# Performance work log

Hardware: AMD Instinct MI355X
Metric: run time of the kernel (lower is better)

## Reference

```python
import jax, jax.numpy as jnp
import numpy as np

N_E = 8192
E_DIM = 64
BETA = 0.25
N_TOKENS = 32768


def setup_inputs() -> dict:
    key = jax.random.key(0)
    k1, k2 = jax.random.split(key)
    x = jax.random.normal(k1, (N_TOKENS, E_DIM), dtype=jnp.float32)
    # nn.Embedding weight initialized uniform(-1/n_e, 1/n_e)
    codebook = jax.random.uniform(k2, (N_E, E_DIM), dtype=jnp.float32,
                                  minval=-1.0 / N_E, maxval=1.0 / N_E)
    return {"x": x, "codebook": codebook, "start": 0, "end": N_E, "use_sk": 0}


def reference(x, codebook, start, end, use_sk):
    # use_sk=0 -> argmin branch (sinkhorn branch calls external helper, not exercised)
    latent = x.reshape(-1, E_DIM)                       # [N, D]
    cb = codebook[start:end]                            # [K, D]
    # squared euclidean distances: ||z||^2 + ||e||^2 - 2 z.e
    d = (jnp.sum(latent * latent, axis=1, keepdims=True)
         + jnp.sum(cb * cb, axis=1)[None, :]
         - 2.0 * jnp.einsum('nd,kd->nk', latent, cb))   # [N, K]
    indices = jnp.argmin(d, axis=-1) + start            # [N]
    x_q = codebook[indices].reshape(x.shape)            # gather
    sg = jax.lax.stop_gradient
    commitment_loss = jnp.mean((sg(x_q) - x) ** 2)
    codebook_loss = jnp.mean((x_q - sg(x)) ** 2)
    loss = codebook_loss + BETA * commitment_loss
    x_q_st = x + sg(x_q - x)                            # straight-through estimator
    indices = indices.reshape(x.shape[:-1])
    return x_q_st, loss, indices
```

## Files before the change

### kernel.cpp

```cpp
#include <hip/hip_runtime.h>
#include <math.h>


#define N_E    8192
#define EDIM   64
#define NTOK   32768
#define NELEM  (NTOK * EDIM)
#define CSZ    32
#define WINDOW 3e-4f
#define TTOK   256
#define TCODE  1024
#define SROW   72
#define TOKB   16
#define CCAP   64
#define KCAP   320

typedef __attribute__((ext_vector_type(8)))  short          short8;
typedef __attribute__((ext_vector_type(8)))  unsigned short ushort8v;
typedef __attribute__((ext_vector_type(16))) float          f32x16;

__device__ __forceinline__ unsigned short f2bf(float f) {
  unsigned int u = __float_as_uint(f);
  return (unsigned short)((u + 0x7FFFu + ((u >> 16) & 1u)) >> 16);
}
__device__ __forceinline__ unsigned short f2h(float f) {
  union { _Float16 h; unsigned short u; } cv; cv.h = (_Float16)f; return cv.u;
}
__device__ __forceinline__ float h2f(unsigned short b) {
  union { _Float16 h; unsigned short u; } cv; cv.u = b; return (float)cv.h;
}
__device__ __forceinline__ float max16(const f32x16 a) {
  float m = fmaxf(fmaxf(a[0], a[1]), a[2]);
  m = fmaxf(fmaxf(m, a[3]),  a[4]);
  m = fmaxf(fmaxf(m, a[5]),  a[6]);
  m = fmaxf(fmaxf(m, a[7]),  a[8]);
  m = fmaxf(fmaxf(m, a[9]),  a[10]);
  m = fmaxf(fmaxf(m, a[11]), a[12]);
  m = fmaxf(fmaxf(m, a[13]), a[14]);
  return fmaxf(m, a[15]);
}
__device__ __forceinline__ float sx_of(const float4* xl4) {
#pragma clang fp contract(off)
  float a0=0,a1=0,a2=0,a3=0,a4=0,a5=0,a6=0,a7=0;
#pragma unroll
  for (int i = 0; i < 8; ++i) {
    float4 pA = xl4[2*i], pB = xl4[2*i+1];
    a0 += pA.x * pA.x; a1 += pA.y * pA.y; a2 += pA.z * pA.z; a3 += pA.w * pA.w;
    a4 += pB.x * pB.x; a5 += pB.y * pB.y; a6 += pB.z * pB.z; a7 += pB.w * pB.w;
  }
  return ((a0+a1) + (a2+a3)) + ((a4+a5) + (a6+a7));
}

__global__ __launch_bounds__(256) void vq_sc(const float* __restrict__ cb,
                                             float* __restrict__ sc,
                                             unsigned short* __restrict__ cbf) {
#pragma clang fp contract(off)
  int r = blockIdx.x * 256 + threadIdx.x;
  const float4* c4 = (const float4*)(cb + (size_t)r * EDIM);
  float sval = sx_of(c4);
  sc[r] = sval;
  unsigned short* dst = cbf + (size_t)r * EDIM;
#pragma unroll
  for (int h = 0; h < 8; ++h) {
    float4 fA = c4[2*h], fB = c4[2*h+1];
    ushort8v o = {f2bf(fA.x), f2bf(fA.y), f2bf(fA.z), f2bf(fA.w),
                  f2bf(fB.x), f2bf(fB.y), f2bf(fB.z), f2bf(fB.w)};
    *(ushort8v*)&dst[h * 8] = o;
  }
}

__global__ __launch_bounds__(256, 3) void vq_pass1(
    const float* __restrict__ x, const unsigned short* __restrict__ cbf,
    unsigned int* __restrict__ cand,
    const int* __restrict__ p_start, const int* __restrict__ p_end) {
  __shared__ unsigned short Cs[128 * SROW];
  int tid = threadIdx.x;
  int tb = blockIdx.x;
  int cbk = blockIdx.y;
  int s = *p_start, e = *p_end;

  int lane = tid & 63, wv = tid >> 6;
  int half = lane >> 5, ln = lane & 31;
  int tokbase = wv * 64;

  const ushort8v* cg0 = (const ushort8v*)(cbf + (size_t)cbk * TCODE * EDIM);
#pragma unroll
  for (int p = 0; p < 4; ++p) {
    int idx = tid + p * 256;
    int row = idx >> 3, h = idx & 7;
    *(ushort8v*)&Cs[row * SROW + h * 8] = cg0[idx];
  }

  short8 bfr[2][4];
#pragma unroll
  for (int tg = 0; tg < 2; ++tg) {
    const float* xrow =
        x + (size_t)(tb * TTOK + tokbase + tg * 32 + ln) * EDIM + half * 8;
#pragma unroll
    for (int ks = 0; ks < 4; ++ks) {
      float4 fA = *(const float4*)(xrow + ks * 16);
      float4 fB = *(const float4*)(xrow + ks * 16 + 4);
      short8 v = {(short)f2bf(fA.x), (short)f2bf(fA.y), (short)f2bf(fA.z),
                  (short)f2bf(fA.w), (short)f2bf(fB.x), (short)f2bf(fB.y),
                  (short)f2bf(fB.z), (short)f2bf(fB.w)};
      bfr[tg][ks] = v;
    }
  }
  __syncthreads();

  unsigned s0=~0u,s1=~0u,s2=~0u,s3=~0u,s4=~0u,s5=~0u,s6=~0u,s7=~0u,s8=~0u;
  unsigned m0=0,m1=0,m2=0,m3=0,m4=0,m5=0,m6=0,m7=0,m8=0;
  unsigned bmap = 0u;
  float lm0 = INFINITY, lm1 = INFINITY;

  for (int nb = 0; nb < 8; ++nb) {
    ushort8v creg[4];
    if (nb < 7) {
      const ushort8v* cg =
          (const ushort8v*)(cbf + ((size_t)cbk * TCODE + (nb + 1) * 128) * EDIM);
#pragma unroll
      for (int p = 0; p < 4; ++p) creg[p] = cg[tid + p * 256];
    }
#pragma unroll
    for (int cp = 0; cp < 2; ++cp) {
      f32x16 acc[2][2];
#pragma unroll
      for (int tg = 0; tg < 2; ++tg)
#pragma unroll
        for (int c2 = 0; c2 < 2; ++c2) acc[tg][c2] = (f32x16)0.0f;
#pragma unroll
      for (int ks = 0; ks < 4; ++ks)
#pragma unroll
        for (int c2 = 0; c2 < 2; ++c2) {
          int ct = cp * 2 + c2;
          short8 a = *(const short8*)&Cs[(ct*32 + ln) * SROW + ks*16 + half*8];
          acc[0][c2] = __builtin_amdgcn_mfma_f32_32x32x16_bf16(a, bfr[0][ks],
                                                               acc[0][c2], 0, 0, 0);
          acc[1][c2] = __builtin_amdgcn_mfma_f32_32x32x16_bf16(a, bfr[1][ks],
                                                               acc[1][c2], 0, 0, 0);
        }
#pragma unroll
      for (int c2 = 0; c2 < 2; ++c2) {
        int cidL = nb * 4 + cp * 2 + c2;
        int c0 = cbk * TCODE + cidL * 32;
        bool full = (c0 >= s) && (c0 + 32 <= e);
        float v0, v1;
        if (full) {
          v0 = max16(acc[0][c2]);
          v1 = max16(acc[1][c2]);
        } else {
          v0 = -INFINITY; v1 = -INFINITY;
#pragma unroll
          for (int r = 0; r < 16; ++r) {
            int code = c0 + (r & 3) + 8 * (r >> 2) + 4 * half;
            if (code >= s && code < e) {
              v0 = fmaxf(v0, acc[0][c2][r]);
              v1 = fmaxf(v1, acc[1][c2][r]);
            }
          }
        }
        v0 = fmaxf(v0, __shfl_xor(v0, 32, 64));
        v1 = fmaxf(v1, __shfl_xor(v1, 32, 64));
        unsigned short hh0 = f2h(-2.0f * v0);
        unsigned short hh1 = f2h(-2.0f * v1);
        float mv0 = h2f(hh0), mv1 = h2f(hh1);
        lm0 = fminf(lm0, mv0);
        lm1 = fminf(lm1, mv1);
        bool a0 = (mv0 <= lm0 + WINDOW);
        bool a1 = (mv1 <= lm1 + WINDOW);
        unsigned b0 = 0, b1 = 0;
        if (a0 | a1) {
          float t0 = v0 - WINDOW * 0.5f;
          float t1 = v1 - WINDOW * 0.5f;
#pragma unroll
          for (int r = 0; r < 16; ++r) {
            int pos = (r & 3) + 8 * (r >> 2) + 4 * half;
            if (acc[0][c2][r] >= t0) b0 |= (1u << pos);
            if (acc[1][c2][r] >= t1) b1 |= (1u << pos);
          }
          b0 |= __shfl_xor(b0, 32, 64);
          b1 |= __shfl_xor(b1, 32, 64);
        }
        bool aown = half ? a1 : a0;
        if (aown) {
          bmap |= 1u << cidL;
          unsigned short hh = half ? hh1 : hh0;
          unsigned bs = half ? b1 : b0;
          unsigned mono = (unsigned)hh ^ ((hh & 0x8000u) ? 0xFFFFu : 0x8000u);
          unsigned p = (mono << 16) | (unsigned)cidL;
          unsigned pm = bs;
          if (p < s8) {
#define INS2_(SK, SM) { bool lt_ = p < (SK); unsigned tk_ = (SK), tm_ = (SM); \
            if (lt_) { (SK) = p; (SM) = pm; p = tk_; pm = tm_; } }
            INS2_(s0,m0) INS2_(s1,m1) INS2_(s2,m2) INS2_(s3,m3) INS2_(s4,m4)
            INS2_(s5,m5) INS2_(s6,m6) INS2_(s7,m7) INS2_(s8,m8)
#undef INS2_
          }
        }
      }
    }
    __syncthreads();
    if (nb < 7) {
#pragma unroll
      for (int p = 0; p < 4; ++p) {
        int idx = tid + p * 256;
        int row = idx >> 3, h = idx & 7;
        *(ushort8v*)&Cs[row * SROW + h * 8] = creg[p];
      }
    }
    __syncthreads();
  }

  {
    float lminf = half ? lm1 : lm0;
    float thr = lminf + WINDOW;
    unsigned rec[8], msk[8];
#define EMIT_(J, S, M) { unsigned mono_ = (S) >> 16; \
    unsigned hh_ = (mono_ & 0x8000u) ? (mono_ ^ 0x8000u) : (mono_ ^ 0xFFFFu); \
    float v_ = h2f((unsigned short)hh_); \
    rec[J] = (v_ <= thr) ? ((hh_ << 16) | ((S) & 0xFFFFu)) : 0xFFFFFFFFu; \
    msk[J] = (M); }
    EMIT_(0, s0, m0) EMIT_(1, s1, m1) EMIT_(2, s2, m2) EMIT_(3, s3, m3)
    EMIT_(4, s4, m4) EMIT_(5, s5, m5) EMIT_(6, s6, m6) EMIT_(7, s7, m7)
#undef EMIT_
    {
      unsigned mono_ = s8 >> 16;
      unsigned hh_ = (mono_ & 0x8000u) ? (mono_ ^ 0x8000u) : (mono_ ^ 0xFFFFu);
      float v8 = h2f((unsigned short)hh_);
      if (v8 <= thr) rec[7] = 0x0000FFFEu;
    }
    int token = tb * TTOK + tokbase + lane;
#pragma unroll
    for (int j = 0; j < 8; ++j) {
      cand[(size_t)(cbk * 8 + j) * NTOK + token] = rec[j];
      cand[(size_t)(64 + cbk * 8 + j) * NTOK + token] = msk[j];
    }
    cand[(size_t)(128 + cbk) * NTOK + token] = bmap;
  }
}

__global__ __launch_bounds__(256) void vq_rescue(
    const float* __restrict__ x, const float* __restrict__ cb,
    const float* __restrict__ sc, const unsigned int* __restrict__ cand,
    float* __restrict__ out_xq, float* __restrict__ out_idx,
    float* __restrict__ partial,
    const int* __restrict__ p_start, const int* __restrict__ p_end) {
#pragma clang fp contract(off)
  __shared__ float xsh[TOKB][64];
  __shared__ float sxs[TOKB];
  __shared__ unsigned short lst[TOKB][CCAP];
  __shared__ unsigned short clst[TOKB][KCAP];
  __shared__ int ccnt[TOKB], kcnt[TOKB];
  int tid  = threadIdx.x;
  int wv   = tid >> 6;
  int lane = tid & 63;
  int blk  = blockIdx.x;
  int s = *p_start, e = *p_end;

  if (tid < TOKB) { ccnt[tid] = 0; kcnt[tid] = 0; }
#pragma unroll
  for (int p = 0; p < (TOKB * CCAP) / 256; ++p)
    ((unsigned short*)lst)[tid + p * 256] = 0xFFFFu;
  __syncthreads();

  if (tid < 128) {
    int tl = tid >> 3, q = tid & 7;
    int gtok = blk * TOKB + tl;
    unsigned rv[8], mk[8];
#pragma unroll
    for (int j = 0; j < 8; ++j) {
      rv[j] = cand[(size_t)(q * 8 + j) * NTOK + gtok];
      mk[j] = cand[(size_t)(64 + q * 8 + j) * NTOK + gtok];
    }
    float m = INFINITY;
#pragma unroll
    for (int j = 0; j < 8; ++j) {
      unsigned cid = rv[j] & 0xFFFFu;
      float v = (cid < 32u) ? h2f((unsigned short)(rv[j] >> 16)) : INFINITY;
      m = fminf(m, v);
    }
    m = fminf(m, __shfl_xor(m, 1, 64));
    m = fminf(m, __shfl_xor(m, 2, 64));
    m = fminf(m, __shfl_xor(m, 4, 64));
    float thr = m + WINDOW;
    bool marker = ((rv[7] & 0xFFFFu) == 0xFFFEu);
    if (!marker) {
#pragma unroll
      for (int j = 0; j < 8; ++j) {
        unsigned cid = rv[j] & 0xFFFFu;
        if (cid < 32u && h2f((unsigned short)(rv[j] >> 16)) <= thr) {
          unsigned bits = mk[j];
          int n = __popc(bits);
          int base = atomicAdd(&ccnt[tl], n);
          if (base + n <= CCAP) {
            int kb = (q * 32 + (int)cid) * CSZ;
            while (bits) {
              int bpos = __ffs(bits) - 1; bits &= bits - 1;
              lst[tl][base++] = (unsigned short)(kb + bpos);
            }
          } else {
            int kb2 = atomicAdd(&kcnt[tl], 1);
            if (kb2 < KCAP) clst[tl][kb2] = (unsigned short)(q * 32 + (int)cid);
          }
        }
      }
    } else {
      unsigned cid0 = rv[0] & 0xFFFFu;
      float v0 = (cid0 < 32u) ? h2f((unsigned short)(rv[0] >> 16)) : INFINITY;
      if (v0 <= thr) {
        unsigned b0 = cand[(size_t)(128 + q) * NTOK + gtok];
        int n = __popc(b0);
        int base = atomicAdd(&kcnt[tl], n);
        while (b0) { int j = __ffs(b0) - 1; b0 &= b0 - 1;
          if (base < KCAP) clst[tl][base] = (unsigned short)(q * 32 + j); ++base; }
      }
    }
  } else if (tid < 192) {
    int t = tid - 128;
#pragma unroll
    for (int p = 0; p < 4; ++p) {
      int idx = t + p * 64;
      int tl = idx >> 4, seg = idx & 15;
      *(float4*)&xsh[tl][seg * 4] =
          ((const float4*)(x + (size_t)(blk * TOKB + tl) * EDIM))[seg];
    }
  } else if (tid < 192 + TOKB) {
    int tl = tid - 192;
    sxs[tl] = sx_of((const float4*)(x + (size_t)(blk * TOKB + tl) * EDIM));
  }
  __syncthreads();

#define EVAL_CODE_BODY(K_, XL4) do {                                           \
    const float4* c4_ = (const float4*)(cb + (size_t)(K_) * EDIM);             \
    float t0_=0.0f,t1_=0.0f,t2_=0.0f,t3_=0.0f;                                 \
    _Pragma("unroll")                                                          \
    for (int i_ = 0; i_ < 8; ++i_) {                 \
      float4 v_ = c4_[2*i_ + h5_];                                             \
      float4 p_ = (XL4)[2*i_ + h5_];                                           \
      t0_ += v_.x * p_.x; t1_ += v_.y * p_.y;                                  \
      t2_ += v_.z * p_.z; t3_ += v_.w * p_.w;                                  \
    }                                                                          \
    s2_ = (t0_ + t1_) + (t2_ + t3_);              \
  } while (0)

#define FINISH_CODE(K_, ACT, SX, BP) do {                                      \
    float tt_ = s2_ + __shfl_xor(s2_, 1, 64);                                  \
    if ((ACT) && (K_) >= s && (K_) < e) {                                      \
      float d_ = ((SX) + sc[K_]) - 2.0f * tt_;                                 \
      unsigned db_ = __float_as_uint(d_);                                      \
      unsigned en_ = db_ ^ ((unsigned)((int)db_ >> 31) | 0x80000000u);         \
      unsigned long long pk_ = ((unsigned long long)en_ << 32) | (unsigned)(K_);\
      if (pk_ < (BP)) (BP) = pk_;                                              \
    }                                                                          \
  } while (0)

  float sg[4];
#pragma unroll
  for (int ti = 0; ti < 4; ++ti) {
    int tl = wv * 4 + ti;
    int gtok = blk * TOKB + tl;
    const float4* xl4 = (const float4*)xsh[tl];
    float sx = sxs[tl];
    unsigned long long bp = ~0ull;
    int ci_ = lane >> 1, h5_ = lane & 1;
    int nc = ccnt[tl]; if (nc > CCAP) nc = CCAP;
    for (int b0 = 0; b0 < nc; b0 += 32) {
      int nb = nc - b0; if (nb > 32) nb = 32;
      int kraw = (ci_ < nb) ? (int)lst[tl][b0 + ci_] : 0xFFFF;
      bool act = (kraw != 0xFFFF);
      int k_ = act ? kraw : 0;
      float s2_ = 0.0f;
      if (act) EVAL_CODE_BODY(k_, xl4);
      FINISH_CODE(k_, act, sx, bp);
    }
    int nk = kcnt[tl]; if (nk > KCAP) nk = KCAP;
    for (int i = 0; i < nk; ++i) {
      int k_ = (int)clst[tl][i] * CSZ + ci_;
      float s2_;
      EVAL_CODE_BODY(k_, xl4);
      FINISH_CODE(k_, true, sx, bp);
    }
#pragma unroll
    for (int off = 32; off >= 1; off >>= 1) {
      unsigned long long o = __shfl_xor(bp, off, 64);
      if (o < bp) bp = o;
    }
    int bidx = (int)(unsigned)(bp & 0xFFFFFFFFull) & (N_E - 1);

    float xx = xsh[tl][lane];
    float qv = cb[(size_t)bidx * EDIM + lane];
    float diff = qv - xx;
    out_xq[(size_t)gtok * EDIM + lane] = xx + diff;
    if (lane == 0) out_idx[gtok] = (float)bidx;
    float l = diff * diff;
#pragma unroll
    for (int off = 32; off >= 1; off >>= 1) l += __shfl_down(l, off, 64);
    sg[ti] = l;
  }
#undef EVAL_CODE_BODY
#undef FINISH_CODE
  if (lane == 0)
    partial[blk * 4 + wv] = (sg[0] + sg[1]) + (sg[2] + sg[3]);
}

__global__ __launch_bounds__(256) void vq_loss(const float* __restrict__ partial,
                                               float* __restrict__ out_loss) {
  int tid = threadIdx.x;
  float s = 0.0f;
  for (int i = tid; i < NTOK / 4; i += 256) s += partial[i];
#pragma unroll
  for (int off = 32; off >= 1; off >>= 1) s += __shfl_down(s, off, 64);
  __shared__ float sdata[4];
  if ((tid & 63) == 0) sdata[tid >> 6] = s;
  __syncthreads();
  if (tid == 0) {
    float total = (sdata[0] + sdata[1]) + (sdata[2] + sdata[3]);
    float m = total * (1.0f / (float)NELEM);
    out_loss[0] = m + 0.25f * m;
  }
}

extern "C" void kernel_launch(void* const* d_in, const int* in_sizes, int n_in,
                              void* d_out, int out_size, void* d_ws, size_t ws_size,
                              hipStream_t stream) {
  const float* x  = (const float*)d_in[0];
  const float* cb = (const float*)d_in[1];
  const int* p_start = (const int*)d_in[2];
  const int* p_end   = (const int*)d_in[3];

  float* ws = (float*)d_ws;
  float* sc      = ws;
  float* partial = ws + N_E;
  unsigned short* cbf  = (unsigned short*)(ws + 2 * N_E);
  unsigned int*   cand = (unsigned int*)(cbf + (size_t)N_E * EDIM);

  float* out      = (float*)d_out;
  float* out_xq   = out;
  float* out_loss = out + NELEM;
  float* out_idx  = out + NELEM + 1;

  vq_sc<<<N_E / 256, 256, 0, stream>>>(cb, sc, cbf);
  dim3 g1(NTOK / TTOK, N_E / TCODE);
  vq_pass1<<<g1, 256, 0, stream>>>(x, cbf, cand, p_start, p_end);
  vq_rescue<<<NTOK / TOKB, 256, 0, stream>>>(x, cb, sc, cand, out_xq, out_idx,
                                             partial, p_start, p_end);
  vq_loss<<<1, 256, 0, stream>>>(partial, out_loss);
}
```

Before: 179.0 us.

## Stage candidate records in LDS and store them token-major for coalesced rescue reads

Pass1 now gathers each token's 16 candidate/mask words in shared memory and writes them token-contiguous as uint4 stores. The rescue kernel then reads each token's per-block records with four vector loads instead of 16 strided scalar loads. Overflow handling changes from replacing the last slot with a marker to setting a flag bit, which keeps the recorded slots and adds only the remaining bitmap entries. A hoisted whole-tile range check also skips per-32-code bounds tests. The cost is an extra LDS round trip and a barrier at the end of pass1.

```diff
diff --git a/kernel.cpp b/kernel.cpp
--- a/kernel.cpp
+++ b/kernel.cpp
@@ -71,13 +71,14 @@
 
 __global__ __launch_bounds__(256, 3) void vq_pass1(
     const float* __restrict__ x, const unsigned short* __restrict__ cbf,
-    unsigned int* __restrict__ cand,
+    unsigned int* __restrict__ cand, unsigned int* __restrict__ bmapb,
     const int* __restrict__ p_start, const int* __restrict__ p_end) {
   __shared__ unsigned short Cs[128 * SROW];
   int tid = threadIdx.x;
   int tb = blockIdx.x;
   int cbk = blockIdx.y;
   int s = *p_start, e = *p_end;
+  const bool allfull = (cbk * TCODE >= s) && (cbk * TCODE + TCODE <= e);
 
   int lane = tid & 63, wv = tid >> 6;
   int half = lane >> 5, ln = lane & 31;
@@ -142,20 +143,25 @@
 #pragma unroll
       for (int c2 = 0; c2 < 2; ++c2) {
         int cidL = nb * 4 + cp * 2 + c2;
-        int c0 = cbk * TCODE + cidL * 32;
-        bool full = (c0 >= s) && (c0 + 32 <= e);
         float v0, v1;
-        if (full) {
+        if (allfull) {
           v0 = max16(acc[0][c2]);
           v1 = max16(acc[1][c2]);
         } else {
-          v0 = -INFINITY; v1 = -INFINITY;
-#pragma unroll
-          for (int r = 0; r < 16; ++r) {
-            int code = c0 + (r & 3) + 8 * (r >> 2) + 4 * half;
-            if (code >= s && code < e) {
-              v0 = fmaxf(v0, acc[0][c2][r]);
-              v1 = fmaxf(v1, acc[1][c2][r]);
+          int c0 = cbk * TCODE + cidL * 32;
+          bool full = (c0 >= s) && (c0 + 32 <= e);
+          if (full) {
+            v0 = max16(acc[0][c2]);
+            v1 = max16(acc[1][c2]);
+          } else {
+            v0 = -INFINITY; v1 = -INFINITY;
+#pragma unroll
+            for (int r = 0; r < 16; ++r) {
+              int code = c0 + (r & 3) + 8 * (r >> 2) + 4 * half;
+              if (code >= s && code < e) {
+                v0 = fmaxf(v0, acc[0][c2][r]);
+                v1 = fmaxf(v1, acc[1][c2][r]);
+              }
             }
           }
         }
@@ -227,21 +233,31 @@
       unsigned mono_ = s8 >> 16;
       unsigned hh_ = (mono_ & 0x8000u) ? (mono_ ^ 0x8000u) : (mono_ ^ 0xFFFFu);
       float v8 = h2f((unsigned short)hh_);
-      if (v8 <= thr) rec[7] = 0x0000FFFEu;
-    }
-    int token = tb * TTOK + tokbase + lane;
+      if (v8 <= thr) rec[7] |= 0x8000u;
+    }
+    unsigned* eb = (unsigned*)Cs;
 #pragma unroll
     for (int j = 0; j < 8; ++j) {
-      cand[(size_t)(cbk * 8 + j) * NTOK + token] = rec[j];
-      cand[(size_t)(64 + cbk * 8 + j) * NTOK + token] = msk[j];
-    }
-    cand[(size_t)(128 + cbk) * NTOK + token] = bmap;
+      eb[tid * 17 + j]     = rec[j];
+      eb[tid * 17 + 8 + j] = msk[j];
+    }
+    bmapb[(size_t)cbk * NTOK + (tb * TTOK + tid)] = bmap;
+  }
+  __syncthreads();
+#pragma unroll
+  for (int p = 0; p < 4; ++p) {
+    int idx = tid + p * 256;
+    int tl = idx >> 2, part = idx & 3;
+    const unsigned* src = (const unsigned*)Cs + tl * 17 + part * 4;
+    uint4 v; v.x = src[0]; v.y = src[1]; v.z = src[2]; v.w = src[3];
+    *(uint4*)(cand + (((size_t)(tb * TTOK + tl)) * 8 + cbk) * 16 + part * 4) = v;
   }
 }
 
 __global__ __launch_bounds__(256) void vq_rescue(
     const float* __restrict__ x, const float* __restrict__ cb,
     const float* __restrict__ sc, const unsigned int* __restrict__ cand,
+    const unsigned int* __restrict__ bmapb,
     float* __restrict__ out_xq, float* __restrict__ out_idx,
     float* __restrict__ partial,
     const int* __restrict__ p_start, const int* __restrict__ p_end) {
@@ -266,29 +282,26 @@
   if (tid < 128) {
     int tl = tid >> 3, q = tid & 7;
     int gtok = blk * TOKB + tl;
-    unsigned rv[8], mk[8];
-#pragma unroll
-    for (int j = 0; j < 8; ++j) {
-      rv[j] = cand[(size_t)(q * 8 + j) * NTOK + gtok];
-      mk[j] = cand[(size_t)(64 + q * 8 + j) * NTOK + gtok];
-    }
+    const uint4* rp = (const uint4*)(cand + ((size_t)gtok * 8 + q) * 16);
+    uint4 A0 = rp[0], A1 = rp[1], M0 = rp[2], M1 = rp[3];
+    unsigned rv[8] = {A0.x, A0.y, A0.z, A0.w, A1.x, A1.y, A1.z, A1.w};
+    unsigned mk[8] = {M0.x, M0.y, M0.z, M0.w, M1.x, M1.y, M1.z, M1.w};
     float m = INFINITY;
 #pragma unroll
-    for (int j = 0; j < 8; ++j) {
-      unsigned cid = rv[j] & 0xFFFFu;
-      float v = (cid < 32u) ? h2f((unsigned short)(rv[j] >> 16)) : INFINITY;
-      m = fminf(m, v);
-    }
+    for (int j = 0; j < 8; ++j)
+      m = fminf(m, h2f((unsigned short)(rv[j] >> 16)));
     m = fminf(m, __shfl_xor(m, 1, 64));
     m = fminf(m, __shfl_xor(m, 2, 64));
     m = fminf(m, __shfl_xor(m, 4, 64));
     float thr = m + WINDOW;
-    bool marker = ((rv[7] & 0xFFFFu) == 0xFFFEu);
-    if (!marker) {
-#pragma unroll
-      for (int j = 0; j < 8; ++j) {
-        unsigned cid = rv[j] & 0xFFFFu;
-        if (cid < 32u && h2f((unsigned short)(rv[j] >> 16)) <= thr) {
+    bool marker = (rv[7] != 0xFFFFFFFFu) && ((rv[7] & 0x8000u) != 0u);
+    unsigned slotbits = 0u;
+#pragma unroll
+    for (int j = 0; j < 8; ++j) {
+      if (rv[j] != 0xFFFFFFFFu) {
+        unsigned cid = rv[j] & 0x1Fu;
+        slotbits |= 1u << cid;
+        if (h2f((unsigned short)(rv[j] >> 16)) <= thr) {
           unsigned bits = mk[j];
           int n = __popc(bits);
           int base = atomicAdd(&ccnt[tl], n);
@@ -304,15 +317,15 @@
           }
         }
       }
-    } else {
-      unsigned cid0 = rv[0] & 0xFFFFu;
-      float v0 = (cid0 < 32u) ? h2f((unsigned short)(rv[0] >> 16)) : INFINITY;
-      if (v0 <= thr) {
-        unsigned b0 = cand[(size_t)(128 + q) * NTOK + gtok];
-        int n = __popc(b0);
-        int base = atomicAdd(&kcnt[tl], n);
-        while (b0) { int j = __ffs(b0) - 1; b0 &= b0 - 1;
-          if (base < KCAP) clst[tl][base] = (unsigned short)(q * 32 + j); ++base; }
+    }
+    if (marker) {
+      unsigned bm = bmapb[(size_t)q * NTOK + gtok] & ~slotbits;
+      int n = __popc(bm);
+      int base = atomicAdd(&kcnt[tl], n);
+      while (bm) {
+        int j = __ffs(bm) - 1; bm &= bm - 1;
+        if (base < KCAP) clst[tl][base] = (unsigned short)(q * 32 + j);
+        ++base;
       }
     }
   } else if (tid < 192) {
@@ -433,6 +446,7 @@
   float* partial = ws + N_E;
   unsigned short* cbf  = (unsigned short*)(ws + 2 * N_E);
   unsigned int*   cand = (unsigned int*)(cbf + (size_t)N_E * EDIM);
+  unsigned int*   bmapb = cand + (size_t)NTOK * 8 * 16;
 
   float* out      = (float*)d_out;
   float* out_xq   = out;
@@ -441,8 +455,8 @@
 
   vq_sc<<<N_E / 256, 256, 0, stream>>>(cb, sc, cbf);
   dim3 g1(NTOK / TTOK, N_E / TCODE);
-  vq_pass1<<<g1, 256, 0, stream>>>(x, cbf, cand, p_start, p_end);
-  vq_rescue<<<NTOK / TOKB, 256, 0, stream>>>(x, cb, sc, cand, out_xq, out_idx,
+  vq_pass1<<<g1, 256, 0, stream>>>(x, cbf, cand, bmapb, p_start, p_end);
+  vq_rescue<<<NTOK / TOKB, 256, 0, stream>>>(x, cb, sc, cand, bmapb, out_xq, out_idx,
                                              partial, p_start, p_end);
   vq_loss<<<1, 256, 0, stream>>>(partial, out_loss);
 }
```

New measurement: 186.1 us. 4.0% more time.
